# Kernel tuning notes

Hardware: AMD Instinct MI355X
Metric: run time of the kernel (lower is better)

The kernel has to match this reference:

```python
import jax, jax.numpy as jnp
import numpy as np
from jax import lax

LAM = 1.0   # risk.distance calls wasserstein with lam=1
ITS = 20    # and its=20
EPS_K = 1e-6


def setup_inputs() -> dict:
    key = jax.random.key(0)
    k1, k2 = jax.random.split(key)
    N, S, D = 4096, 32, 128
    X_ls = jax.random.normal(k1, (N, S, D), dtype=jnp.float32)
    t = jax.random.randint(k2, (N,), 0, 2).astype(jnp.int32)
    return {"X_ls": X_ls, "t": t}


def _pdist2sq(X, Y):
    # squared Euclidean distance between all pairs: [nt, nc]
    C = -2.0 * (X @ Y.T)
    nx = jnp.sum(jnp.square(X), axis=1, keepdims=True)   # [nt,1]
    ny = jnp.sum(jnp.square(Y), axis=1, keepdims=True)   # [nc,1]
    return C + ny.T + nx


def _sinkhorn_step(Xt, Xc, p, lam, its):
    # Xt: [nt, d], Xc: [nc, d]  -> scalar 2*sum(T*Mt)
    nt = jnp.float32(Xt.shape[0])
    nc = jnp.float32(Xc.shape[0])
    M = _pdist2sq(Xt, Xc)                                   # [nt, nc]
    delta = lax.stop_gradient(jnp.max(M))
    eff_lam = lax.stop_gradient(lam / jnp.mean(M))
    # augmented cost matrix Mt: [nt+1, nc+1]
    row = delta * jnp.ones((1, M.shape[1]), M.dtype)
    col = jnp.concatenate([delta * jnp.ones((M.shape[0], 1), M.dtype),
                           jnp.zeros((1, 1), M.dtype)], axis=0)
    Mt = jnp.concatenate([jnp.concatenate([M, row], axis=0), col], axis=1)
    # marginals a: [nt+1,1], b: [nc+1,1]
    a = jnp.concatenate([(p / nt) * jnp.ones((Xt.shape[0], 1), M.dtype),
                         (1.0 - p) * jnp.ones((1, 1), M.dtype)], axis=0)
    b = jnp.concatenate([((1.0 - p) / nc) * jnp.ones((Xc.shape[0], 1), M.dtype),
                         p * jnp.ones((1, 1), M.dtype)], axis=0)
    K = jnp.exp(-eff_lam * Mt) + EPS_K
    ainvK = K / a
    def body(i, u):
        # u^T K -> transpose -> K^T u : [nc+1,1]
        return 1.0 / (ainvK @ (b / (K.T @ u)))
    u = lax.fori_loop(0, its, body, a)
    v = b / (K.T @ u)                                       # [nc+1,1]
    T = u * (v.T * K)                                       # [nt+1, nc+1]
    T = lax.stop_gradient(T)                                # backpropT=False
    return 2.0 * jnp.sum(T * Mt)


def _wasserstein(X_ls, t, lam=LAM, its=ITS):
    # Data-dependent split on treatment (concrete, eager) — matches tf.where+gather.
    t_np = np.asarray(t)
    it_idx = np.nonzero(t_np > 0)[0]
    ic_idx = np.nonzero(t_np < 1)[0]
    p = jnp.float32(t_np.astype(np.float32).mean())          # p_t = np.mean(t)
    Xt_all = jnp.transpose(X_ls[it_idx], (1, 0, 2))          # [S, nt, d]
    Xc_all = jnp.transpose(X_ls[ic_idx], (1, 0, 2))          # [S, nc, d]
    per_step = jax.vmap(lambda Xt, Xc: _sinkhorn_step(Xt, Xc, p, lam, its))
    return jnp.sum(per_step(Xt_all, Xc_all))                 # sum over timesteps


def reference(X_ls, t):
    return _wasserstein(X_ls, t)
```

## Files before the change

kernel.cpp:

```cpp
#include <hip/hip_runtime.h>
#include <stdint.h>

typedef unsigned char u8;
typedef unsigned short u16;
typedef uint32_t u32;

#define NTOT 4096
#define SS   32
#define DD   128
#define EPSK 1e-6f
#define NITER 20
#define CAPC 4460544u
#define LDC_FIT 2304
#define WSTR 2432
#define SU_OFF 2308
#define UNT_OFF 2309
#define BPT 16

typedef __attribute__((ext_vector_type(8))) short short8;
typedef __attribute__((ext_vector_type(4))) float f32x4;
typedef __attribute__((ext_vector_type(2))) float f32x2;

__device__ __forceinline__ float bf2f(u16 h){ return __uint_as_float(((u32)h) << 16); }
__device__ __forceinline__ u16 f2bf(float f){
  u32 u = __float_as_uint(f);
  u += 0x7fffu + ((u >> 16) & 1u);
  return (u16)(u >> 16);
}
__device__ __forceinline__ int invpermc(int cp){
  return (cp & ~63) | ((cp & 3) << 4) | ((cp >> 2) & 15);
}

__global__ __launch_bounds__(1024) void k_compact(const int* __restrict__ t,
    int* __restrict__ itidx, int* __restrict__ icidx, int* __restrict__ meta,
    float* __restrict__ fmeta)
{
  __shared__ int sc[1024];
  int tid = threadIdx.x;
  int e0 = tid * 4;
  int tv[4]; int c = 0;
  #pragma unroll
  for (int e = 0; e < 4; e++){ tv[e] = t[e0 + e]; c += (tv[e] > 0) ? 1 : 0; }
  sc[tid] = c;
  __syncthreads();
  for (int off = 1; off < 1024; off <<= 1){
    int v = sc[tid];
    int add = (tid >= off) ? sc[tid - off] : 0;
    __syncthreads();
    sc[tid] = v + add;
    __syncthreads();
  }
  int incl = sc[tid];
  int excl = incl - c;
  int oT = excl, oC = e0 - excl;
  #pragma unroll
  for (int e = 0; e < 4; e++){
    if (tv[e] > 0) itidx[oT++] = e0 + e;
    else           icidx[oC++] = e0 + e;
  }
  if (tid == 1023){
    meta[0] = incl; meta[1] = NTOT - incl;
    fmeta[0] = (float)incl / (float)NTOT;
  }
}

__global__ void k_zero(float* __restrict__ p, int n)
{
  int i = blockIdx.x * 256 + threadIdx.x;
  if (i < n) p[i] = 0.f;
}

__global__ void k_vinit(const float* __restrict__ fmeta, float* __restrict__ w0)
{
  if (threadIdx.x == 0){
    float p = fmeta[0];
    float* w = w0 + (size_t)blockIdx.x * WSTR;
    w[SU_OFF]  = p;
    w[UNT_OFF] = 1.0f - p;
  }
}

__global__ __launch_bounds__(256) void k_pack(const float* __restrict__ X,
    const int* __restrict__ itidx, const int* __restrict__ icidx,
    const int* __restrict__ meta, u16* __restrict__ XT, u16* __restrict__ XC,
    float* __restrict__ nxT, float* __restrict__ nxC, int ts0)
{
  int r = blockIdx.x * 256 + threadIdx.x;
  int isC = blockIdx.y;
  int z = blockIdx.z;
  int s = ts0 + z;
  int n = isC ? meta[1] : meta[0];
  if (r >= n) return;
  int idx = isC ? icidx[r] : itidx[r];
  const float4* src = (const float4*)(X + ((size_t)idx * SS + s) * DD);
  u16* dst = (isC ? XC : XT) + ((size_t)z * NTOT + r) * DD;
  float nrm = 0.f;
  #pragma unroll
  for (int q = 0; q < 32; q++){
    float4 v = src[q];
    nrm += v.x*v.x + v.y*v.y + v.z*v.z + v.w*v.w;
    u32 lo = (u32)f2bf(v.x) | ((u32)f2bf(v.y) << 16);
    u32 hi = (u32)f2bf(v.z) | ((u32)f2bf(v.w) << 16);
    uint2 pk; pk.x = lo; pk.y = hi;
    ((uint2*)dst)[q] = pk;
  }
  (isC ? nxC : nxT)[z * NTOT + r] = nrm;
}

__global__ __launch_bounds__(256) void k_stats(const u16* __restrict__ XT,
    const u16* __restrict__ XC, const float* __restrict__ nxT, const float* __restrict__ nxC,
    const int* __restrict__ meta, float* __restrict__ gsx, float* __restrict__ gsn)
{
  int side = blockIdx.y, z = blockIdx.z;
  int n = side ? meta[1] : meta[0];
  int chunk = (n + 7) >> 3;
  int r0 = blockIdx.x * chunk;
  int r1 = min(r0 + chunk, n);
  const u16* B = (side ? XC : XT) + (size_t)z * NTOT * DD;
  int tid = threadIdx.x;
  int d = tid & 127, half = tid >> 7;
  float sx = 0.f;
  for (int r = r0 + half; r < r1; r += 2) sx += bf2f(B[(size_t)r * DD + d]);
  __shared__ float sp[256];
  sp[tid] = sx;
  __syncthreads();
  if (tid < 128) unsafeAtomicAdd(&gsx[(size_t)(z*2+side)*128 + tid], sp[tid] + sp[tid+128]);
  const float* nrm = (side ? nxC : nxT) + (size_t)z * NTOT;
  float sn = 0.f;
  for (int r = r0 + tid; r < r1; r += 256) sn += nrm[r];
  #pragma unroll
  for (int o = 32; o; o >>= 1) sn += __shfl_xor(sn, o);
  __syncthreads();
  if ((tid & 63) == 0) sp[tid >> 6] = sn;
  __syncthreads();
  if (tid == 0) unsafeAtomicAdd(&gsn[z*2+side], sp[0]+sp[1]+sp[2]+sp[3]);
}

__global__ void k_lam(const float* __restrict__ gsx, const float* __restrict__ gsn,
                      const int* __restrict__ meta, float* __restrict__ stats)
{
  int z = blockIdx.x, tid = threadIdx.x;
  float d = gsx[(size_t)(z*2)*128 + tid] * gsx[(size_t)(z*2+1)*128 + tid];
  #pragma unroll
  for (int o = 32; o; o >>= 1) d += __shfl_xor(d, o);
  __shared__ float rr[2];
  if ((tid & 63) == 0) rr[tid >> 6] = d;
  __syncthreads();
  if (tid == 0){
    float nt = (float)meta[0], nc = (float)meta[1];
    float msum = nc * gsn[z*2] + nt * gsn[z*2+1] - 2.f * (rr[0] + rr[1]);
    stats[z*8+0] = nt * nc / msum;
    stats[z*8+1] = msum / (nt * nc);
  }
}

#define LDA2 72
__global__ __launch_bounds__(256) void k_gemm(const u16* __restrict__ XT,
    const u16* __restrict__ XC, const float* __restrict__ nxT, const float* __restrict__ nxC,
    const int* __restrict__ meta, const float* __restrict__ fmeta,
    float* __restrict__ stats, u8* __restrict__ Kc, float* __restrict__ w0base)
{
  int nt = meta[0], nc = meta[1];
  if (nt > LDC_FIT || nc > LDC_FIT) return;
  int bx = blockIdx.x, by = blockIdx.y, z = blockIdx.z;
  if (by * 128 >= nt || bx * 128 >= nc) return;
  __shared__ __align__(16) u16 As[128 * LDA2];
  __shared__ __align__(16) u16 Bs[128 * LDA2];
  __shared__ float watile[256];
  __shared__ float nxs[128];
  __shared__ float nys[128];
  int tid = threadIdx.x;
  int wid = tid >> 6, lane = tid & 63;
  int wm = (wid >> 1) * 64, wn = (wid & 1) * 64;
  int lrow = lane & 15, lquad = lane >> 4;

  if (tid < 128){
    int gi = by*128 + tid;
    nxs[tid] = (gi < nt) ? nxT[(size_t)z * NTOT + gi] : 0.f;
  } else {
    int gj = bx*128 + (tid - 128);
    nys[tid - 128] = (gj < nc) ? nxC[(size_t)z * NTOT + gj] : 0.f;
  }

  f32x4 acc[4][4];
  #pragma unroll
  for (int i = 0; i < 4; i++){
    #pragma unroll
    for (int j = 0; j < 4; j++){
      acc[i][j][0]=0.f; acc[i][j][1]=0.f; acc[i][j][2]=0.f; acc[i][j][3]=0.f;
    }
  }

  int r = tid & 127;
  int isB = tid >> 7;
  int g = (isB ? bx : by) * 128 + r;
  int lim = isB ? nc : nt;
  const u16* srcbase = (isB ? XC : XT) + ((size_t)z * NTOT + g) * DD;
  u16* dl = (isB ? Bs : As) + r * LDA2;

  for (int kh = 0; kh < 2; kh++){
    __syncthreads();
    if (g < lim){
      const uint4* src = (const uint4*)(srcbase + kh * 64);
      #pragma unroll
      for (int q = 0; q < 8; q++) ((uint4*)dl)[q] = src[q];
    } else {
      uint4 zz; zz.x=0; zz.y=0; zz.z=0; zz.w=0;
      #pragma unroll
      for (int q = 0; q < 8; q++) ((uint4*)dl)[q] = zz;
    }
    __syncthreads();
    #pragma unroll
    for (int ks = 0; ks < 2; ks++){
      int koff = ks * 32 + lquad * 8;
      short8 af[4], bfr[4];
      #pragma unroll
      for (int i = 0; i < 4; i++) af[i]  = *(const short8*)(As + (wm + i*16 + lrow) * LDA2 + koff);
      #pragma unroll
      for (int j = 0; j < 4; j++) bfr[j] = *(const short8*)(Bs + (wn + j*16 + lrow) * LDA2 + koff);
      #pragma unroll
      for (int i = 0; i < 4; i++){
        #pragma unroll
        for (int j = 0; j < 4; j++){
          acc[i][j] = __builtin_amdgcn_mfma_f32_16x16x32_bf16(af[i], bfr[j], acc[i][j], 0, 0, 0);
        }
      }
    }
  }

  int ldc = (nc + 127) & ~127;
  float lam = stats[z*8+0];
  float p = fmeta[0];
  float a0 = p / (float)nt;
  u8* Kz = Kc + (size_t)z * CAPC;

  float nyv[4]; bool jin[4];
  #pragma unroll
  for (int j = 0; j < 4; j++){
    int lcol = wn + j*16 + lrow;
    jin[j] = (bx*128 + lcol) < nc;
    nyv[j] = nys[lcol];
  }
  float vmax = 0.f;
  float colsum[4] = {0.f, 0.f, 0.f, 0.f};
  size_t cbase = (size_t)(bx*128 + wn + lrow*4);
  #pragma unroll
  for (int i = 0; i < 4; i++){
    #pragma unroll
    for (int rr2 = 0; rr2 < 4; rr2++){
      int lr = wm + i*16 + lquad*4 + rr2;
      int gi = by*128 + lr;
      bool iin = gi < nt;
      float nxv = nxs[lr];
      float cv[4];
      #pragma unroll
      for (int j = 0; j < 4; j++){
        float m = nxv + nyv[j] - 2.0f * acc[i][j][rr2];
        cv[j] = __expf(-lam * m);
        if (iin && jin[j]){ vmax = fmaxf(vmax, m); colsum[j] += cv[j]; }
      }
      u32 pk = (u32)__builtin_amdgcn_cvt_pk_fp8_f32(cv[0], cv[1], 0, false);
      pk = (u32)__builtin_amdgcn_cvt_pk_fp8_f32(cv[2], cv[3], (int)pk, true);
      if (iin) *(u32*)(Kz + (size_t)gi * ldc + cbase) = pk;
    }
  }
  #pragma unroll
  for (int j = 0; j < 4; j++){
    colsum[j] += __shfl_xor(colsum[j], 16);
    colsum[j] += __shfl_xor(colsum[j], 32);
  }
  if (lane < 16){
    #pragma unroll
    for (int j = 0; j < 4; j++) watile[wid * 64 + j*16 + lrow] = colsum[j];
  }
  #pragma unroll
  for (int o = 32; o; o >>= 1) vmax = fmaxf(vmax, __shfl_xor(vmax, o));
  if (lane == 0) atomicMax((int*)stats + z*8 + 2, __float_as_int(vmax));
  __syncthreads();
  if (tid < 128){
    int gj = bx*128 + tid;
    if (gj < nc){
      float v = (tid < 64) ? (watile[tid] + watile[128 + tid])
                           : (watile[64 + (tid-64)] + watile[192 + (tid-64)]);
      unsafeAtomicAdd(w0base + (size_t)z * WSTR + gj, v * a0);
    }
  }
}

__global__ __launch_bounds__(256, 2) void k_iter(const u8* __restrict__ Kc,
    const float* __restrict__ wprev, float* __restrict__ wnext,
    float* __restrict__ ubuf, const int* __restrict__ meta,
    const float* __restrict__ fmeta, const float* __restrict__ stats, int writeU)
{
  __shared__ __align__(16) float zl[LDC_FIT];
  __shared__ __align__(16) float watw[4 * LDC_FIT];
  __shared__ float red[4];
  int nt = meta[0], nc = meta[1];
  if (nt > LDC_FIT || nc > LDC_FIT) return;
  int ldc = (nc + 127) & ~127;
  int z = blockIdx.y, b = blockIdx.x;
  int tid = threadIdx.x, wid = tid >> 6, lane = tid & 63;
  float p = fmeta[0];
  float b0 = (1.0f - p) / (float)nc;
  float a0 = p / (float)nt;
  float lam = stats[z*8+0];
  float delta = stats[z*8+2];
  float kc = __expf(-lam * delta);
  float kce = kc + EPSK;
  const float* wp = wprev + (size_t)z * WSTR;
  float* wnx = wnext + (size_t)z * WSTR;
  float SU = wp[SU_OFF], UNT = wp[UNT_OFF];
  float wext = EPSK * (SU + UNT) + kc * UNT;
  float wnc = kce * SU + (1.0f + EPSK) * UNT;
  float znc = p / wnc;

  float zp = 0.f;
  for (int cp = tid; cp < ldc; cp += 256){
    int c = invpermc(cp);
    float v = 0.f;
    if (c < nc) v = b0 * __builtin_amdgcn_rcpf(wp[c] + wext);
    zl[cp] = v;
    zp += v;
  }
  #pragma unroll
  for (int o = 32; o; o >>= 1) zp += __shfl_xor(zp, o);
  if (lane == 0) red[wid] = zp;
  __syncthreads();
  float Z = red[0] + red[1] + red[2] + red[3];
  float dotX = EPSK * Z + kce * znc;
  float untN = (1.0f - p) / (kce * Z + (1.0f + EPSK) * znc);

  int cb0 = lane * 16;
  float zv[48];
  #pragma unroll
  for (int s = 0; s < 3; s++){
    int cb = s*1024 + cb0;
    if (cb < ldc){
      #pragma unroll
      for (int q = 0; q < 4; q++){
        float4 t4 = *(const float4*)(zl + cb + q*4);
        zv[s*16+q*4+0]=t4.x; zv[s*16+q*4+1]=t4.y; zv[s*16+q*4+2]=t4.z; zv[s*16+q*4+3]=t4.w;
      }
    } else {
      #pragma unroll
      for (int k = 0; k < 16; k++) zv[s*16+k] = 0.f;
    }
  }

  float wacc[48];
  #pragma unroll
  for (int k = 0; k < 48; k++) wacc[k] = 0.f;
  float rsum = 0.f;

  int rpb = (nt + BPT - 1) / BPT;
  int r0 = b * rpb, r1 = min(r0 + rpb, nt);
  const u8* Kz = Kc + (size_t)z * CAPC;

  for (int r = r0 + wid; r < r1; r += 4){
    const u8* Kr = Kz + (size_t)r * ldc;
    uint4 kq[3];
    #pragma unroll
    for (int s = 0; s < 3; s++){
      int cb = s*1024 + cb0;
      if (cb < ldc) kq[s] = *(const uint4*)(Kr + cb);
      else { kq[s].x=0u; kq[s].y=0u; kq[s].z=0u; kq[s].w=0u; }
    }
    float kd[48];
    #pragma unroll
    for (int s = 0; s < 3; s++){
      u32 wd[4] = {kq[s].x, kq[s].y, kq[s].z, kq[s].w};
      #pragma unroll
      for (int q = 0; q < 4; q++){
        f32x2 d0 = __builtin_amdgcn_cvt_pk_f32_fp8((int)wd[q], false);
        f32x2 d1 = __builtin_amdgcn_cvt_pk_f32_fp8((int)wd[q], true);
        kd[s*16+q*4+0] = d0.x; kd[s*16+q*4+1] = d0.y;
        kd[s*16+q*4+2] = d1.x; kd[s*16+q*4+3] = d1.y;
      }
    }
    float d4[4] = {0.f, 0.f, 0.f, 0.f};
    #pragma unroll
    for (int k = 0; k < 48; k++) d4[k & 3] = fmaf(kd[k], zv[k], d4[k & 3]);
    float dot = (d4[0] + d4[1]) + (d4[2] + d4[3]);
    #pragma unroll
    for (int o = 32; o; o >>= 1) dot += __shfl_xor(dot, o);
    float uv = a0 * __builtin_amdgcn_rcpf(dot + dotX);
    rsum += uv;
    if (writeU && lane == 0) ubuf[(size_t)z * WSTR + r] = uv;
    #pragma unroll
    for (int k = 0; k < 48; k++) wacc[k] = fmaf(kd[k], uv, wacc[k]);
  }
  #pragma unroll
  for (int s = 0; s < 3; s++){
    int cb = s*1024 + cb0;
    if (cb < ldc){
      #pragma unroll
      for (int q = 0; q < 4; q++)
        *(float4*)(watw + (size_t)wid * LDC_FIT + cb + q*4) =
            make_float4(wacc[s*16+q*4+0], wacc[s*16+q*4+1], wacc[s*16+q*4+2], wacc[s*16+q*4+3]);
    }
  }
  if (lane == 0) unsafeAtomicAdd(wnx + SU_OFF, rsum);
  if (b == 0 && tid == 0) wnx[UNT_OFF] = untN;
  __syncthreads();
  for (int cp = tid; cp < ldc; cp += 256){
    int c = invpermc(cp);
    if (c < nc){
      float v = watw[cp] + watw[LDC_FIT + cp] + watw[2*LDC_FIT + cp] + watw[3*LDC_FIT + cp];
      unsafeAtomicAdd(wnx + c, v);
    }
  }
}

__global__ __launch_bounds__(256, 2) void k_fin(const u8* __restrict__ Kc,
    const float* __restrict__ wprev, const float* __restrict__ ubuf,
    const int* __restrict__ meta, const float* __restrict__ fmeta,
    const float* __restrict__ stats, float* __restrict__ tsacc, int ts0)
{
  __shared__ __align__(16) float zl[LDC_FIT];
  __shared__ float red[4];
  int nt = meta[0], nc = meta[1];
  if (nt > LDC_FIT || nc > LDC_FIT) return;
  int ldc = (nc + 127) & ~127;
  int z = blockIdx.y, b = blockIdx.x;
  int tid = threadIdx.x, wid = tid >> 6, lane = tid & 63;
  float p = fmeta[0];
  float b0 = (1.0f - p) / (float)nc;
  float lam = stats[z*8+0];
  float invlam = stats[z*8+1];
  float delta = stats[z*8+2];
  float kc = __expf(-lam * delta);
  float kce = kc + EPSK;
  const float* wp = wprev + (size_t)z * WSTR;
  float SU = wp[SU_OFF], UNT = wp[UNT_OFF];
  float wext = EPSK * (SU + UNT) + kc * UNT;
  float wnc = kce * SU + (1.0f + EPSK) * UNT;
  float znc = p / wnc;

  float zp = 0.f;
  for (int cp = tid; cp < ldc; cp += 256){
    int c = invpermc(cp);
    float v = 0.f;
    if (c < nc) v = b0 * __builtin_amdgcn_rcpf(wp[c] + wext);
    zl[cp] = v;
    zp += v;
  }
  #pragma unroll
  for (int o = 32; o; o >>= 1) zp += __shfl_xor(zp, o);
  if (lane == 0) red[wid] = zp;
  __syncthreads();
  float Z = red[0] + red[1] + red[2] + red[3];

  int cb0 = lane * 16;
  float zv[48];
  #pragma unroll
  for (int s = 0; s < 3; s++){
    int cb = s*1024 + cb0;
    if (cb < ldc){
      #pragma unroll
      for (int q = 0; q < 4; q++){
        float4 t4 = *(const float4*)(zl + cb + q*4);
        zv[s*16+q*4+0]=t4.x; zv[s*16+q*4+1]=t4.y; zv[s*16+q*4+2]=t4.z; zv[s*16+q*4+3]=t4.w;
      }
    } else {
      #pragma unroll
      for (int k = 0; k < 16; k++) zv[s*16+k] = 0.f;
    }
  }

  int rpb = (nt + BPT - 1) / BPT;
  int r0 = b * rpb, r1 = min(r0 + rpb, nt);
  const u8* Kz = Kc + (size_t)z * CAPC;
  float wsum = 0.f;

  for (int r = r0 + wid; r < r1; r += 4){
    const u8* Kr = Kz + (size_t)r * ldc;
    float d4[4] = {0.f, 0.f, 0.f, 0.f};
    #pragma unroll
    for (int s = 0; s < 3; s++){
      int cb = s*1024 + cb0;
      if (cb < ldc){
        uint4 kq = *(const uint4*)(Kr + cb);
        u32 wd[4] = {kq.x, kq.y, kq.z, kq.w};
        #pragma unroll
        for (int q = 0; q < 4; q++){
          f32x2 d0 = __builtin_amdgcn_cvt_pk_f32_fp8((int)wd[q], false);
          f32x2 d1 = __builtin_amdgcn_cvt_pk_f32_fp8((int)wd[q], true);
          float cc[4] = {d0.x, d0.y, d1.x, d1.y};
          int k0 = s*16+q*4;
          #pragma unroll
          for (int e = 0; e < 4; e++){
            d4[e] = fmaf((cc[e] + EPSK) * zv[k0+e], __logf(fmaxf(cc[e], 1e-4f)), d4[e]);
          }
        }
      }
    }
    float inner = (d4[0] + d4[1]) + (d4[2] + d4[3]);
    #pragma unroll
    for (int o = 32; o; o >>= 1) inner += __shfl_xor(inner, o);
    wsum += ubuf[(size_t)z * WSTR + r] * inner;
  }
  if (lane == 0) unsafeAtomicAdd(tsacc + ts0 + z, -invlam * wsum);
  if (b == 0 && tid == 0){
    float aug = delta * kce * (UNT * Z + SU * znc);
    unsafeAtomicAdd(tsacc + ts0 + z, aug);
  }
}

__global__ void k_out(const float* __restrict__ tsacc, float* __restrict__ out)
{
  if (threadIdx.x == 0){
    float s = 0.f;
    for (int i = 0; i < SS; i++) s += tsacc[i];
    out[0] = 2.0f * s;
  }
}

extern "C" void kernel_launch(void* const* d_in, const int* in_sizes, int n_in,
                              void* d_out, int out_size, void* d_ws, size_t ws_size,
                              hipStream_t stream)
{
  const float* X = (const float*)d_in[0];
  const int* t = (const int*)d_in[1];

  const size_t PER_TS = 6810000u;
  const size_t FIXED  = 262144u;
  int TSG = 1;
  if (ws_size > FIXED + PER_TS){
    size_t g = (ws_size - FIXED) / PER_TS;
    TSG = (g > SS) ? SS : (int)g;
  }

  char* pp = (char*)d_ws;
  auto alloc = [&](size_t bytes) -> void* {
    void* r = (void*)pp;
    pp += (bytes + 255) & ~(size_t)255;
    return r;
  };
  u8*    Kbuf  = (u8*)alloc((size_t)TSG * CAPC);
  u16*   XT    = (u16*)alloc((size_t)TSG * NTOT * DD * 2);
  u16*   XC    = (u16*)alloc((size_t)TSG * NTOT * DD * 2);
  float* nxT   = (float*)alloc((size_t)TSG * NTOT * 4);
  float* nxC   = (float*)alloc((size_t)TSG * NTOT * 4);
  float* wbuf  = (float*)alloc((size_t)(NITER + 1) * TSG * WSTR * 4);
  float* ubuf  = (float*)alloc((size_t)TSG * WSTR * 4);
  float* auxf  = (float*)alloc((size_t)TSG * 272 * 4);
  int*   itidx = (int*)alloc(NTOT * 4);
  int*   icidx = (int*)alloc(NTOT * 4);
  int*   meta  = (int*)alloc(256);
  float* fmeta = (float*)alloc(256);
  float* tsacc = (float*)alloc(256);

  float* gsx   = auxf;
  float* gsn   = auxf + (size_t)TSG*256;
  float* stats = gsn + (size_t)TSG*2;
  const int auxn = TSG * 266;
  const int wn  = (NITER + 1) * TSG * WSTR;

  k_zero<<<1, 256, 0, stream>>>(tsacc, 64);
  k_compact<<<1, 1024, 0, stream>>>(t, itidx, icidx, meta, fmeta);

  for (int ts0 = 0; ts0 < SS; ts0 += TSG){
    int cnt = SS - ts0; if (cnt > TSG) cnt = TSG;

    k_zero<<<(auxn + 255)/256, 256, 0, stream>>>(auxf, auxn);
    k_zero<<<(wn + 255)/256, 256, 0, stream>>>(wbuf, wn);
    k_vinit<<<cnt, 64, 0, stream>>>(fmeta, wbuf);
    k_pack<<<dim3(16, 2, cnt), 256, 0, stream>>>(X, itidx, icidx, meta, XT, XC, nxT, nxC, ts0);
    k_stats<<<dim3(8, 2, cnt), 256, 0, stream>>>(XT, XC, nxT, nxC, meta, gsx, gsn);
    k_lam<<<cnt, 128, 0, stream>>>(gsx, gsn, meta, stats);
    k_gemm<<<dim3(18, 18, cnt), 256, 0, stream>>>(XT, XC, nxT, nxC, meta, fmeta, stats, Kbuf, wbuf);

    for (int it = 0; it < NITER; it++){
      k_iter<<<dim3(BPT, cnt), 256, 0, stream>>>(Kbuf,
          wbuf + (size_t)it * TSG * WSTR,
          wbuf + (size_t)(it + 1) * TSG * WSTR,
          ubuf, meta, fmeta, stats, (it == NITER - 1) ? 1 : 0);
    }
    k_fin<<<dim3(BPT, cnt), 256, 0, stream>>>(Kbuf,
        wbuf + (size_t)NITER * TSG * WSTR, ubuf, meta, fmeta, stats, tsacc, ts0);
  }
  k_out<<<1, 64, 0, stream>>>(tsacc, (float*)d_out);
}
```

Measured before the change: 1.221 ms.

## Software-prefetch next K row, recompute fp8 decode, raise occupancy and blocks

Sinkhorn iteration and final kernels now load the next row's fp8 K data into registers while the current row is processed, hiding global load latency. The 48-float decoded row array is dropped in favour of decoding twice from the packed words, which cuts register pressure so launch bounds can move from 2 to 3 blocks per SM. Blocks per timestep rise from 16 to 24. The trade is extra conversion instructions and more atomic partial-sum traffic from the added blocks.

```diff
diff --git a/kernel.cpp b/kernel.cpp
--- a/kernel.cpp
+++ b/kernel.cpp
@@ -15,7 +15,7 @@
 #define WSTR 2432
 #define SU_OFF 2308
 #define UNT_OFF 2309
-#define BPT 16
+#define BPT 24
 
 typedef __attribute__((ext_vector_type(8))) short short8;
 typedef __attribute__((ext_vector_type(4))) float f32x4;
@@ -30,6 +30,7 @@
 __device__ __forceinline__ int invpermc(int cp){
   return (cp & ~63) | ((cp & 3) << 4) | ((cp >> 2) & 15);
 }
+__device__ __forceinline__ uint4 u4zero(){ uint4 t; t.x=0u; t.y=0u; t.z=0u; t.w=0u; return t; }
 
 __global__ __launch_bounds__(1024) void k_compact(const int* __restrict__ t,
     int* __restrict__ itidx, int* __restrict__ icidx, int* __restrict__ meta,
@@ -287,7 +288,7 @@
   }
 }
 
-__global__ __launch_bounds__(256, 2) void k_iter(const u8* __restrict__ Kc,
+__global__ __launch_bounds__(256, 3) void k_iter(const u8* __restrict__ Kc,
     const float* __restrict__ wprev, float* __restrict__ wnext,
     float* __restrict__ ubuf, const int* __restrict__ meta,
     const float* __restrict__ fmeta, const float* __restrict__ stats, int writeU)
@@ -356,30 +357,38 @@
   int r0 = b * rpb, r1 = min(r0 + rpb, nt);
   const u8* Kz = Kc + (size_t)z * CAPC;
 
-  for (int r = r0 + wid; r < r1; r += 4){
+  bool c0ok = (cb0 < ldc), c1ok = (1024 + cb0 < ldc), c2ok = (2048 + cb0 < ldc);
+  uint4 kq0 = u4zero(), kq1 = u4zero(), kq2 = u4zero();
+  int r = r0 + wid;
+  if (r < r1){
     const u8* Kr = Kz + (size_t)r * ldc;
-    uint4 kq[3];
-    #pragma unroll
-    for (int s = 0; s < 3; s++){
-      int cb = s*1024 + cb0;
-      if (cb < ldc) kq[s] = *(const uint4*)(Kr + cb);
-      else { kq[s].x=0u; kq[s].y=0u; kq[s].z=0u; kq[s].w=0u; }
-    }
-    float kd[48];
-    #pragma unroll
-    for (int s = 0; s < 3; s++){
-      u32 wd[4] = {kq[s].x, kq[s].y, kq[s].z, kq[s].w};
-      #pragma unroll
-      for (int q = 0; q < 4; q++){
-        f32x2 d0 = __builtin_amdgcn_cvt_pk_f32_fp8((int)wd[q], false);
-        f32x2 d1 = __builtin_amdgcn_cvt_pk_f32_fp8((int)wd[q], true);
-        kd[s*16+q*4+0] = d0.x; kd[s*16+q*4+1] = d0.y;
-        kd[s*16+q*4+2] = d1.x; kd[s*16+q*4+3] = d1.y;
-      }
-    }
+    if (c0ok) kq0 = *(const uint4*)(Kr + cb0);
+    if (c1ok) kq1 = *(const uint4*)(Kr + 1024 + cb0);
+    if (c2ok) kq2 = *(const uint4*)(Kr + 2048 + cb0);
+  }
+  for (; r < r1; r += 4){
+    uint4 kn0 = u4zero(), kn1 = u4zero(), kn2 = u4zero();
+    int rn = r + 4;
+    if (rn < r1){
+      const u8* Krn = Kz + (size_t)rn * ldc;
+      if (c0ok) kn0 = *(const uint4*)(Krn + cb0);
+      if (c1ok) kn1 = *(const uint4*)(Krn + 1024 + cb0);
+      if (c2ok) kn2 = *(const uint4*)(Krn + 2048 + cb0);
+    }
+    u32 wd[12] = {kq0.x, kq0.y, kq0.z, kq0.w,
+                  kq1.x, kq1.y, kq1.z, kq1.w,
+                  kq2.x, kq2.y, kq2.z, kq2.w};
     float d4[4] = {0.f, 0.f, 0.f, 0.f};
     #pragma unroll
-    for (int k = 0; k < 48; k++) d4[k & 3] = fmaf(kd[k], zv[k], d4[k & 3]);
+    for (int q = 0; q < 12; q++){
+      f32x2 e0 = __builtin_amdgcn_cvt_pk_f32_fp8((int)wd[q], false);
+      f32x2 e1 = __builtin_amdgcn_cvt_pk_f32_fp8((int)wd[q], true);
+      int k0 = q * 4;
+      d4[0] = fmaf(e0.x, zv[k0+0], d4[0]);
+      d4[1] = fmaf(e0.y, zv[k0+1], d4[1]);
+      d4[2] = fmaf(e1.x, zv[k0+2], d4[2]);
+      d4[3] = fmaf(e1.y, zv[k0+3], d4[3]);
+    }
     float dot = (d4[0] + d4[1]) + (d4[2] + d4[3]);
     #pragma unroll
     for (int o = 32; o; o >>= 1) dot += __shfl_xor(dot, o);
@@ -387,7 +396,16 @@
     rsum += uv;
     if (writeU && lane == 0) ubuf[(size_t)z * WSTR + r] = uv;
     #pragma unroll
-    for (int k = 0; k < 48; k++) wacc[k] = fmaf(kd[k], uv, wacc[k]);
+    for (int q = 0; q < 12; q++){
+      f32x2 e0 = __builtin_amdgcn_cvt_pk_f32_fp8((int)wd[q], false);
+      f32x2 e1 = __builtin_amdgcn_cvt_pk_f32_fp8((int)wd[q], true);
+      int k0 = q * 4;
+      wacc[k0+0] = fmaf(e0.x, uv, wacc[k0+0]);
+      wacc[k0+1] = fmaf(e0.y, uv, wacc[k0+1]);
+      wacc[k0+2] = fmaf(e1.x, uv, wacc[k0+2]);
+      wacc[k0+3] = fmaf(e1.y, uv, wacc[k0+3]);
+    }
+    kq0 = kn0; kq1 = kn1; kq2 = kn2;
   }
   #pragma unroll
   for (int s = 0; s < 3; s++){
@@ -411,7 +429,7 @@
   }
 }
 
-__global__ __launch_bounds__(256, 2) void k_fin(const u8* __restrict__ Kc,
+__global__ __launch_bounds__(256, 3) void k_fin(const u8* __restrict__ Kc,
     const float* __restrict__ wprev, const float* __restrict__ ubuf,
     const int* __restrict__ meta, const float* __restrict__ fmeta,
     const float* __restrict__ stats, float* __restrict__ tsacc, int ts0)
@@ -472,32 +490,43 @@
   const u8* Kz = Kc + (size_t)z * CAPC;
   float wsum = 0.f;
 
-  for (int r = r0 + wid; r < r1; r += 4){
+  bool c0ok = (cb0 < ldc), c1ok = (1024 + cb0 < ldc), c2ok = (2048 + cb0 < ldc);
+  uint4 kq0 = u4zero(), kq1 = u4zero(), kq2 = u4zero();
+  int r = r0 + wid;
+  if (r < r1){
     const u8* Kr = Kz + (size_t)r * ldc;
+    if (c0ok) kq0 = *(const uint4*)(Kr + cb0);
+    if (c1ok) kq1 = *(const uint4*)(Kr + 1024 + cb0);
+    if (c2ok) kq2 = *(const uint4*)(Kr + 2048 + cb0);
+  }
+  for (; r < r1; r += 4){
+    uint4 kn0 = u4zero(), kn1 = u4zero(), kn2 = u4zero();
+    int rn = r + 4;
+    if (rn < r1){
+      const u8* Krn = Kz + (size_t)rn * ldc;
+      if (c0ok) kn0 = *(const uint4*)(Krn + cb0);
+      if (c1ok) kn1 = *(const uint4*)(Krn + 1024 + cb0);
+      if (c2ok) kn2 = *(const uint4*)(Krn + 2048 + cb0);
+    }
+    u32 wd[12] = {kq0.x, kq0.y, kq0.z, kq0.w,
+                  kq1.x, kq1.y, kq1.z, kq1.w,
+                  kq2.x, kq2.y, kq2.z, kq2.w};
     float d4[4] = {0.f, 0.f, 0.f, 0.f};
     #pragma unroll
-    for (int s = 0; s < 3; s++){
-      int cb = s*1024 + cb0;
-      if (cb < ldc){
-        uint4 kq = *(const uint4*)(Kr + cb);
-        u32 wd[4] = {kq.x, kq.y, kq.z, kq.w};
-        #pragma unroll
-        for (int q = 0; q < 4; q++){
-          f32x2 d0 = __builtin_amdgcn_cvt_pk_f32_fp8((int)wd[q], false);
-          f32x2 d1 = __builtin_amdgcn_cvt_pk_f32_fp8((int)wd[q], true);
-          float cc[4] = {d0.x, d0.y, d1.x, d1.y};
-          int k0 = s*16+q*4;
-          #pragma unroll
-          for (int e = 0; e < 4; e++){
-            d4[e] = fmaf((cc[e] + EPSK) * zv[k0+e], __logf(fmaxf(cc[e], 1e-4f)), d4[e]);
-          }
-        }
-      }
+    for (int q = 0; q < 12; q++){
+      f32x2 e0 = __builtin_amdgcn_cvt_pk_f32_fp8((int)wd[q], false);
+      f32x2 e1 = __builtin_amdgcn_cvt_pk_f32_fp8((int)wd[q], true);
+      int k0 = q * 4;
+      d4[0] = fmaf((e0.x + EPSK) * zv[k0+0], __logf(fmaxf(e0.x, 1e-4f)), d4[0]);
+      d4[1] = fmaf((e0.y + EPSK) * zv[k0+1], __logf(fmaxf(e0.y, 1e-4f)), d4[1]);
+      d4[2] = fmaf((e1.x + EPSK) * zv[k0+2], __logf(fmaxf(e1.x, 1e-4f)), d4[2]);
+      d4[3] = fmaf((e1.y + EPSK) * zv[k0+3], __logf(fmaxf(e1.y, 1e-4f)), d4[3]);
     }
     float inner = (d4[0] + d4[1]) + (d4[2] + d4[3]);
     #pragma unroll
     for (int o = 32; o; o >>= 1) inner += __shfl_xor(inner, o);
     wsum += ubuf[(size_t)z * WSTR + r] * inner;
+    kq0 = kn0; kq1 = kn1; kq2 = kn2;
   }
   if (lane == 0) unsafeAtomicAdd(tsacc + ts0 + z, -invlam * wsum);
   if (b == 0 && tid == 0){
```

Result: slower. 1.584 ms (+29.7%).
